# Kernel optimization log

Measured on AMD Instinct MI355X. Metric: run time of the kernel, lower is better.

The kernel has to match this reference:

```python
import jax, jax.numpy as jnp
import numpy as np
from jax import lax

HID = 128
NGRAPH = 64  # ligands per receptor


def _conv3d(x, w, b):
    # x: [N,C,D,H,W], w: [O,I,3,3,3], VALID padding (torch Conv3d default)
    y = lax.conv_general_dilated(x, w, (1, 1, 1), 'VALID',
                                 dimension_numbers=('NCDHW', 'OIDHW', 'NCDHW'))
    return y + b[None, :, None, None, None]


def setup_inputs() -> dict:
    key = jax.random.key(0)
    ks = jax.random.split(key, 40)
    i = iter(range(40))
    rn = lambda shape, s=1.0: jax.random.normal(ks[next(i)], shape, jnp.float32) * s
    W = 0.02
    inp = {
        'ms_feat_0': rn((4, 32, 16, 16, 16)),
        'ms_feat_1': rn((4, 64, 8, 8, 8)),
        'token_features': rn((4, 128, 256)),
        'lig_atom': rn((4, 1024, 64)),
        'lig_graph': rn((4, NGRAPH, 64)),
        'ligand_batch': jnp.sort(jax.random.randint(ks[next(i)], (1024,), 0, NGRAPH)).astype(jnp.int32),
        # token_mlp
        'W_token': rn((256, HID), W), 'b_token': jnp.zeros((HID,)),
        # pocket_mlp_list (reversed order: conv0 <- ms_feat_1 C=64, conv1 <- ms_feat_0 C=32)
        'Wc0': rn((HID, 64, 3, 3, 3), W), 'bc0': jnp.zeros((HID,)),
        'Wc1': rn((HID, 32, 3, 3, 3), W), 'bc1': jnp.zeros((HID,)),
        # pocket_mlp
        'W_pocket': rn((2 * HID, HID), W), 'b_pocket': jnp.zeros((HID,)),
        # concat layer / gate
        'W_cat': rn((3 * HID, HID), W), 'b_cat': jnp.zeros((HID,)),
        'W_gate': rn((3 * HID, HID), W), 'b_gate': jnp.zeros((HID,)),
        # ligand projections
        'W_atom': rn((64, HID), W), 'b_atom': jnp.zeros((HID,)),
        'W_graph': rn((64, HID), W), 'b_graph': jnp.zeros((HID,)),
        # energy bias mlp
        'W_bias1': rn((2 * HID, HID), W), 'b_bias1': jnp.zeros((HID,)),
        'W_bias2': rn((HID, 1), W), 'b_bias2': jnp.zeros((1,)),
        # interaction mlp + pair energy / gate
        'W_int': rn((HID, HID), W), 'b_int': jnp.zeros((HID,)),
        'W_pe': rn((HID, 1), W), 'b_pe': jnp.zeros((1,)),
        'W_pg': rn((HID, 1), W), 'b_pg': jnp.zeros((1,)),
    }
    return inp


def reference(ms_feat_0, ms_feat_1, token_features, lig_atom, lig_graph, ligand_batch,
              W_token, b_token, Wc0, bc0, Wc1, bc1, W_pocket, b_pocket,
              W_cat, b_cat, W_gate, b_gate, W_atom, b_atom, W_graph, b_graph,
              W_bias1, b_bias1, W_bias2, b_bias2, W_int, b_int,
              W_pe, b_pe, W_pg, b_pg):
    silu = jax.nn.silu
    lrelu = lambda x: jax.nn.leaky_relu(x, 0.01)

    # ---- ready_to_calculate ----
    # reversed multi-scale: [ms_feat_1, ms_feat_0]; SiLU -> Conv3d -> spatial mean
    p0 = _conv3d(silu(ms_feat_1), Wc0, bc0).mean(axis=(2, 3, 4))  # [N,HID]
    p1 = _conv3d(silu(ms_feat_0), Wc1, bc1).mean(axis=(2, 3, 4))  # [N,HID]
    pocket = silu(jnp.concatenate([p0, p1], -1)) @ W_pocket + b_pocket  # [N,HID]

    tok = silu(token_features) @ W_token + b_token                # [N,Nt,HID]
    tok_agg = jnp.concatenate([tok.sum(1), tok.mean(1)], -1)      # [N,2*HID]

    pf = jnp.concatenate([pocket, tok_agg], -1)                   # [N,3*HID]
    pf = (pf @ W_cat + b_cat) * jax.nn.sigmoid(pf @ W_gate + b_gate)  # [N,HID]

    # ---- per-image affinity (vectorized over images) ----
    atoms = lig_atom @ W_atom + b_atom                            # [N,Na,HID]
    # einsum('ik,jk->ijk') outer interaction map, batched over images
    imap = jnp.einsum('nik,njk->nijk', atoms, tok)                # [N,Na,Nt,HID]
    h = lrelu(imap @ W_int + b_int)                               # [N,Na,Nt,HID]
    pe = (h @ W_pe + b_pe) * jax.nn.sigmoid(h @ W_pg + b_pg)      # [N,Na,Nt,1]
    atom_e = pe.sum(axis=(2, 3))                                  # [N,Na]
    seg = jax.vmap(lambda v: jax.ops.segment_sum(v, ligand_batch, num_segments=NGRAPH))(atom_e)  # [N,Ng]

    gf = lig_graph @ W_graph + b_graph                            # [N,Ng,HID]
    pf_rep = jnp.broadcast_to(pf[:, None, :], gf.shape)           # [N,Ng,HID]
    z = jnp.concatenate([pf_rep, gf], -1)                         # [N,Ng,2*HID]
    bias = lrelu(z @ W_bias1 + b_bias1) @ W_bias2 + b_bias2       # [N,Ng,1]

    return seg + bias[..., 0]                                     # [N,Ng]
```

## Files before the change

kernel.cpp:

```cpp
#include <hip/hip_runtime.h>
#include <hip/hip_bf16.h>

#define NIMG 4

typedef __attribute__((ext_vector_type(8))) short short8v;
typedef __attribute__((ext_vector_type(4))) float float4v;

__device__ __forceinline__ float sigm(float x){ return 1.f/(1.f+__expf(-x)); }
__device__ __forceinline__ float silu(float x){ return x/(1.f+__expf(-x)); }
__device__ __forceinline__ float lrelu(float x){ return fmaxf(x, 0.01f*x); }
__device__ __forceinline__ float bf2f(unsigned short u){
  union { unsigned int i; float f; } v; v.i = ((unsigned int)u)<<16; return v.f; }
__device__ __forceinline__ unsigned short f2bf(float f){
  union { float f; unsigned int i; } v; v.f = f;
  unsigned int r = v.i + 0x7fffu + ((v.i>>16)&1u);
  return (unsigned short)(r>>16); }

__global__ void k_tok(const float* __restrict__ tf, const float* __restrict__ Wt,
                      const float* __restrict__ bt, float* __restrict__ tok,
                      float* __restrict__ toksum){
  __shared__ float sv[256];
  __shared__ float part[128];
  const int row = blockIdx.x;
  const int tid = threadIdx.x;
  const int c = tid & 127, s = tid >> 7;
  sv[tid] = silu(tf[row*256 + tid]);
  __syncthreads();
  float acc = 0.f;
  #pragma unroll 8
  for(int q=s*128; q<s*128+128; q++) acc = fmaf(sv[q], Wt[q*128+c], acc);
  if(s==1) part[c] = acc;
  __syncthreads();
  if(s==0){
    acc += part[c] + bt[c];
    tok[row*128+c] = acc;
    atomicAdd(&toksum[(row>>7)*128 + c], acc);
  }
}

template<int DIM, int ODIM>
__global__ void k_wsum(const float* __restrict__ x, float* __restrict__ S){
  __shared__ float sx[DIM*DIM*DIM];
  const float* xp = x + (size_t)blockIdx.x*(DIM*DIM*DIM);
  for(int p=threadIdx.x; p<DIM*DIM*DIM; p+=256) sx[p] = silu(xp[p]);
  __syncthreads();
  const int wave = threadIdx.x>>6, lane = threadIdx.x&63;
  for(int tap=wave; tap<27; tap+=4){
    const int kd=tap/9, kh=(tap/3)%3, kw=tap%3;
    const int base = kd*DIM*DIM + kh*DIM + kw;
    float ps = 0.f;
    for(int idx=lane; idx<ODIM*ODIM*ODIM; idx+=64){
      int od = idx/(ODIM*ODIM); int r = idx - od*(ODIM*ODIM);
      int oh = r/ODIM; int ow = r - oh*ODIM;
      ps += sx[base + od*DIM*DIM + oh*DIM + ow];
    }
    #pragma unroll
    for(int m=32;m>=1;m>>=1) ps += __shfl_xor(ps,m);
    if(lane==0) S[blockIdx.x*27 + tap] = ps;
  }
}

__global__ void k_pconv(const float* __restrict__ S1, const float* __restrict__ S0,
                        const float* __restrict__ Wc0, const float* __restrict__ bc0,
                        const float* __restrict__ Wc1, const float* __restrict__ bc1,
                        float* __restrict__ pp){
  const int b = blockIdx.x;
  const int n = b >> 7, c = b & 127;
  const int tid = threadIdx.x;
  float a0 = 0.f, a1 = 0.f;
  { const float* w = Wc0 + c*1728; const float* s = S1 + n*1728;
    for(int q=tid; q<1728; q+=256) a0 = fmaf(w[q], s[q], a0); }
  { const float* w = Wc1 + c*864;  const float* s = S0 + n*864;
    for(int q=tid; q<864; q+=256)  a1 = fmaf(w[q], s[q], a1); }
  #pragma unroll
  for(int m=32;m>=1;m>>=1){ a0 += __shfl_xor(a0,m); a1 += __shfl_xor(a1,m); }
  __shared__ float r0[4], r1[4];
  if((tid&63)==0){ r0[tid>>6]=a0; r1[tid>>6]=a1; }
  __syncthreads();
  if(tid==0){
    float p0 = bc0[c] + (r0[0]+r0[1]+r0[2]+r0[3])*(1.f/216.f);
    float p1 = bc1[c] + (r1[0]+r1[1]+r1[2]+r1[3])*(1.f/2744.f);
    pp[n*256 + c]       = silu(p0);
    pp[n*256 + 128 + c] = silu(p1);
  }
}

__global__ void k_pf2(const float* __restrict__ pp, const float* __restrict__ toksum,
                      const float* __restrict__ Wp,  const float* __restrict__ bp,
                      const float* __restrict__ Wcat, const float* __restrict__ bcat,
                      const float* __restrict__ Wgate,const float* __restrict__ bgate,
                      float* __restrict__ pf){
  __shared__ float ps[256];
  __shared__ float zz[384];
  __shared__ float part[4][128];
  __shared__ float partg[4][128];
  const int n = blockIdx.x;
  const int tid = threadIdx.x;
  const int c = tid & 127, s = tid >> 7;
  if(tid < 256) ps[tid] = pp[n*256 + tid];
  __syncthreads();
  float a = 0.f;
  for(int q=s*64; q<s*64+64; q++) a = fmaf(ps[q], Wp[q*128+c], a);
  part[s][c] = a;
  __syncthreads();
  if(s==0){
    float pk = bp[c] + part[0][c]+part[1][c]+part[2][c]+part[3][c];
    float ts = toksum[n*128+c];
    zz[c] = pk; zz[128+c] = ts; zz[256+c] = ts*(1.f/128.f);
  }
  __syncthreads();
  float a1=0.f, a2=0.f;
  for(int q=s*96; q<s*96+96; q++){
    float z = zz[q];
    a1 = fmaf(z, Wcat[q*128+c], a1);
    a2 = fmaf(z, Wgate[q*128+c], a2);
  }
  part[s][c]=a1; partg[s][c]=a2;
  __syncthreads();
  if(s==0){
    float v1 = bcat[c] +part[0][c]+part[1][c]+part[2][c]+part[3][c];
    float v2 = bgate[c]+partg[0][c]+partg[1][c]+partg[2][c]+partg[3][c];
    pf[n*128+c] = v1 * sigm(v2);
  }
}

__global__ void k_atoms(const float* __restrict__ la, const float* __restrict__ Wa,
                        const float* __restrict__ ba, unsigned short* __restrict__ atoms_bf,
                        float* __restrict__ atom_e){
  __shared__ float s[64];
  const int row = blockIdx.x;
  const int c = threadIdx.x;
  if(c < 64) s[c] = la[row*64 + c];
  __syncthreads();
  float acc = ba[c];
  #pragma unroll 8
  for(int k=0;k<64;k++) acc = fmaf(s[k], Wa[k*128+c], acc);
  atoms_bf[row*128+c] = f2bf(acc);
  if(c==0) atom_e[row] = 0.f;
}

__global__ void k_wt(const float* __restrict__ Wint, unsigned short* __restrict__ Wt){
  const int c = blockIdx.x, k = threadIdx.x;
  Wt[c*128 + k] = f2bf(Wint[k*128 + c]);
}

__global__ __launch_bounds__(512,2) void k_inter(
    const unsigned short* __restrict__ atoms_bf,
    const float* __restrict__ tok,
    const unsigned short* __restrict__ Wt,
    const float* __restrict__ bint,
    const float* __restrict__ Wpe, const float* __restrict__ bpe,
    const float* __restrict__ Wpg, const float* __restrict__ bpg,
    float* __restrict__ atom_e){
  extern __shared__ unsigned short ldsu[];
  float* red = (float*)(ldsu + 32768);

  const int b0 = blockIdx.x;
  const int bid = (b0 & 7)*64 + (b0 >> 3);
  const int n = bid >> 7;
  const int chunk = (bid >> 5) & 3;
  const int jg = bid & 31;
  const int tid = threadIdx.x;
  const int wv = tid >> 6, lane = tid & 63;
  const int q = lane >> 4, t = lane & 15;
  const int wr = wv >> 1, wc = wv & 1;

  const int rbase = n*1024 + chunk*256;

  short8v areg[4][4];
  const unsigned short* ab = atoms_bf + (size_t)rbase*128 + (wr*64 + t)*128 + q*8;
  #pragma unroll
  for(int fr=0; fr<4; fr++)
    #pragma unroll
    for(int ks=0; ks<4; ks++)
      areg[fr][ks] = *(const short8v*)(ab + fr*16*128 + ks*32);

  const int kq = (tid & 15)*8;
  const int cbb = tid >> 4;
  const int swzW = (cbb & 7) << 3;
  float wf[4][8];
  {
    short8v wtmp[4];
    #pragma unroll
    for(int i=0;i<4;i++) wtmp[i] = *(const short8v*)(Wt + (cbb + 32*i)*128 + kq);
    #pragma unroll
    for(int i=0;i<4;i++)
      #pragma unroll
      for(int e=0;e<8;e++) wf[i][e] = bf2f((unsigned short)wtmp[i][e]);
  }
  const float* tokb = tok + (size_t)(n*128 + jg*4)*128;

  float bi[4], wpe[4], wpg[4];
  #pragma unroll
  for(int fc=0; fc<4; fc++){
    int c = wc*64 + fc*16 + t;
    bi[fc] = bint[c]; wpe[fc] = Wpe[c]; wpg[fc] = Wpg[c];
  }
  const float bpe0 = bpe[0], bpg0 = bpg[0];
  const int swzB = (t & 7) << 3;

  float peacc = 0.f;

  {
    float4v t0 = *(const float4v*)(tokb + kq);
    float4v t1 = *(const float4v*)(tokb + kq + 4);
    float trv[8] = {t0[0],t0[1],t0[2],t0[3],t1[0],t1[1],t1[2],t1[3]};
    #pragma unroll
    for(int i=0;i<4;i++){
      int c = cbb + 32*i;
      short8v o;
      #pragma unroll
      for(int e=0;e<8;e++) o[e] = (short)f2bf(wf[i][e]*trv[e]);
      *(short8v*)(ldsu + (c<<7) + (kq ^ swzW)) = o;
    }
  }
  __syncthreads();

  #pragma unroll
  for(int j=0; j<4; j++){
    float trn[8];
    if(j<3){
      float4v t0 = *(const float4v*)(tokb + (j+1)*128 + kq);
      float4v t1 = *(const float4v*)(tokb + (j+1)*128 + kq + 4);
      #pragma unroll
      for(int e=0;e<4;e++){ trn[e]=t0[e]; trn[4+e]=t1[e]; }
    }
    const unsigned short* B = ldsu + (j&1)*16384;

    float4v acc[4][4];
    #pragma unroll
    for(int fr=0;fr<4;fr++)
      #pragma unroll
      for(int fc=0;fc<4;fc++)
        acc[fr][fc] = (float4v){bi[fc],bi[fc],bi[fc],bi[fc]};

    #pragma unroll
    for(int ks=0;ks<4;ks++){
      #pragma unroll
      for(int fc=0;fc<4;fc++){
        const int c = wc*64 + fc*16 + t;
        short8v bf = *(const short8v*)(B + (c<<7) + ((ks*32 + q*8) ^ swzB));
        #pragma unroll
        for(int fr=0;fr<4;fr++)
          acc[fr][fc] = __builtin_amdgcn_mfma_f32_16x16x32_bf16(areg[fr][ks], bf, acc[fr][fc], 0,0,0);
      }
    }

    #pragma unroll
    for(int fr=0;fr<4;fr++){
      #pragma unroll
      for(int r=0;r<4;r++){
        float d1=0.f, d2=0.f;
        #pragma unroll
        for(int fc=0;fc<4;fc++){
          float h = lrelu(acc[fr][fc][r]);
          d1 = fmaf(h, wpe[fc], d1);
          d2 = fmaf(h, wpg[fc], d2);
        }
        d1 += __shfl_xor(d1,1); d2 += __shfl_xor(d2,1);
        d1 += __shfl_xor(d1,2); d2 += __shfl_xor(d2,2);
        d1 += __shfl_xor(d1,4); d2 += __shfl_xor(d2,4);
        d1 += __shfl_xor(d1,8); d2 += __shfl_xor(d2,8);
        if(t==0){
          int row = wr*64 + fr*16 + q*4 + r;
          red[(wc*256 + row)*2 + 0] = d1;
          red[(wc*256 + row)*2 + 1] = d2;
        }
      }
    }
    __syncthreads();
    if(tid < 256){
      float d1 = red[tid*2]     + red[(256+tid)*2];
      float d2 = red[tid*2 + 1] + red[(256+tid)*2 + 1];
      peacc += (d1 + bpe0) * sigm(d2 + bpg0);
    }
    if(j<3){
      #pragma unroll
      for(int i=0;i<4;i++){
        int c = cbb + 32*i;
        short8v o;
        #pragma unroll
        for(int e=0;e<8;e++) o[e] = (short)f2bf(wf[i][e]*trn[e]);
        *(short8v*)(ldsu + ((j+1)&1)*16384 + (c<<7) + (kq ^ swzW)) = o;
      }
    }
    __syncthreads();
  }
  if(tid < 256) atomicAdd(atom_e + rbase + tid, peacc);
}

__global__ void k_bias_seg(const float* __restrict__ lg, const float* __restrict__ Wg,
                       const float* __restrict__ bg, const float* __restrict__ pf,
                       const float* __restrict__ W1, const float* __restrict__ b1,
                       const float* __restrict__ W2, const float* __restrict__ b2,
                       const float* __restrict__ atom_e, const int* __restrict__ batch,
                       float* __restrict__ out){
  __shared__ float row[64];
  __shared__ float z[256];
  __shared__ float red[128];
  __shared__ float red2[128];
  const int b = blockIdx.x;
  const int n = b >> 6, g = b & 63;
  const int c = threadIdx.x;
  if(c < 64) row[c] = lg[b*64 + c];
  __syncthreads();
  float gf = bg[c];
  #pragma unroll 8
  for(int k=0;k<64;k++) gf = fmaf(row[k], Wg[k*128+c], gf);
  z[c] = pf[n*128+c]; z[128+c] = gf;
  __syncthreads();
  float tacc = b1[c];
  for(int qq=0;qq<256;qq++) tacc = fmaf(z[qq], W1[qq*128+c], tacc);
  tacc = lrelu(tacc);
  float s = 0.f;
  const float* ae = atom_e + n*1024;
  for(int i=c;i<1024;i+=128){ float v = ae[i]; s += (batch[i]==g) ? v : 0.f; }
  red[c] = tacc * W2[c];
  red2[c] = s;
  __syncthreads();
  for(int st=64; st>0; st>>=1){
    if(c<st){ red[c]+=red[c+st]; red2[c]+=red2[c+st]; }
    __syncthreads();
  }
  if(c==0) out[b] = red[0] + b2[0] + red2[0];
}

extern "C" void kernel_launch(void* const* d_in, const int* in_sizes, int n_in,
                              void* d_out, int out_size, void* d_ws, size_t ws_size,
                              hipStream_t stream) {
  const float* ms0   = (const float*)d_in[0];
  const float* ms1   = (const float*)d_in[1];
  const float* tfeat = (const float*)d_in[2];
  const float* la    = (const float*)d_in[3];
  const float* lg    = (const float*)d_in[4];
  const int*   batch = (const int*)  d_in[5];
  const float* Wtok  = (const float*)d_in[6];
  const float* btok  = (const float*)d_in[7];
  const float* Wc0   = (const float*)d_in[8];
  const float* bc0   = (const float*)d_in[9];
  const float* Wc1   = (const float*)d_in[10];
  const float* bc1   = (const float*)d_in[11];
  const float* Wp    = (const float*)d_in[12];
  const float* bp    = (const float*)d_in[13];
  const float* Wcat  = (const float*)d_in[14];
  const float* bcat  = (const float*)d_in[15];
  const float* Wgate = (const float*)d_in[16];
  const float* bgate = (const float*)d_in[17];
  const float* Wa    = (const float*)d_in[18];
  const float* ba    = (const float*)d_in[19];
  const float* Wgr   = (const float*)d_in[20];
  const float* bgr   = (const float*)d_in[21];
  const float* W1    = (const float*)d_in[22];
  const float* b1    = (const float*)d_in[23];
  const float* W2    = (const float*)d_in[24];
  const float* b2    = (const float*)d_in[25];
  const float* Wint  = (const float*)d_in[26];
  const float* bint  = (const float*)d_in[27];
  const float* Wpe   = (const float*)d_in[28];
  const float* bpe   = (const float*)d_in[29];
  const float* Wpg   = (const float*)d_in[30];
  const float* bpg   = (const float*)d_in[31];
  float* out = (float*)d_out;

  float* ws      = (float*)d_ws;
  float* tok     = ws;
  float* S1      = ws + 65536;
  float* S0      = S1 + 6912;
  float* pp      = S0 + 3456;
  float* pf      = pp + 1024;
  float* toksum  = pf + 512;
  float* atom_e  = toksum + 512;
  unsigned short* atoms_bf = (unsigned short*)(atom_e + 4096);
  unsigned short* Wt       = atoms_bf + 524288;

  hipMemsetAsync(toksum, 0, 512*sizeof(float), stream);

  k_tok<<<NIMG*128, 256, 0, stream>>>(tfeat, Wtok, btok, tok, toksum);
  k_wsum<8,6><<<NIMG*64, 256, 0, stream>>>(ms1, S1);
  k_wsum<16,14><<<NIMG*32, 256, 0, stream>>>(ms0, S0);
  k_atoms<<<NIMG*1024, 128, 0, stream>>>(la, Wa, ba, atoms_bf, atom_e);
  k_wt<<<128, 128, 0, stream>>>(Wint, Wt);
  k_pconv<<<NIMG*128, 256, 0, stream>>>(S1, S0, Wc0, bc0, Wc1, bc1, pp);
  k_pf2<<<NIMG, 512, 0, stream>>>(pp, toksum, Wp, bp, Wcat, bcat, Wgate, bgate, pf);

  const int lds_bytes = 65536 + 4096;
  hipFuncSetAttribute(reinterpret_cast<const void*>(k_inter),
                      hipFuncAttributeMaxDynamicSharedMemorySize, lds_bytes);
  k_inter<<<512, 512, lds_bytes, stream>>>(atoms_bf, tok, Wt, bint,
                                           Wpe, bpe, Wpg, bpg, atom_e);

  k_bias_seg<<<NIMG*64, 128, 0, stream>>>(lg, Wgr, bgr, pf, W1, b1, W2, b2,
                                          atom_e, batch, out);
}
```

Measured before the change: 250.1 us.

## Fuse preprocessing kernels and restructure interaction GEMM to scale atom fragments in registers

The tok, wsum, atoms and weight-transpose kernels are merged into one multi-role launch, cutting launch count. The toksum atomics and memset are replaced by a direct column sum inside k_pconv. The interaction kernel no longer builds W*tok tiles in LDS with double buffering and barriers. Instead it keeps W_int fragments in registers and scales the atom A-fragments by each token using packed bf16 conversion. It also uses smaller 256-thread blocks over 64-atom by 8-token tiles and DPP row reductions. The trade-off is extra register pressure and repeated global tok loads per token.

New measurement: 215.5 us. 13.8% less time.

```diff
diff --git a/kernel.cpp b/kernel.cpp
--- a/kernel.cpp
+++ b/kernel.cpp
@@ -5,44 +5,49 @@
 
 typedef __attribute__((ext_vector_type(8))) short short8v;
 typedef __attribute__((ext_vector_type(4))) float float4v;
+typedef __attribute__((ext_vector_type(4))) int   int4v;
 
 __device__ __forceinline__ float sigm(float x){ return 1.f/(1.f+__expf(-x)); }
 __device__ __forceinline__ float silu(float x){ return x/(1.f+__expf(-x)); }
 __device__ __forceinline__ float lrelu(float x){ return fmaxf(x, 0.01f*x); }
-__device__ __forceinline__ float bf2f(unsigned short u){
-  union { unsigned int i; float f; } v; v.i = ((unsigned int)u)<<16; return v.f; }
 __device__ __forceinline__ unsigned short f2bf(float f){
   union { float f; unsigned int i; } v; v.f = f;
   unsigned int r = v.i + 0x7fffu + ((v.i>>16)&1u);
   return (unsigned short)(r>>16); }
 
-__global__ void k_tok(const float* __restrict__ tf, const float* __restrict__ Wt,
-                      const float* __restrict__ bt, float* __restrict__ tok,
-                      float* __restrict__ toksum){
-  __shared__ float sv[256];
-  __shared__ float part[128];
-  const int row = blockIdx.x;
-  const int tid = threadIdx.x;
-  const int c = tid & 127, s = tid >> 7;
-  sv[tid] = silu(tf[row*256 + tid]);
-  __syncthreads();
-  float acc = 0.f;
-  #pragma unroll 8
-  for(int q=s*128; q<s*128+128; q++) acc = fmaf(sv[q], Wt[q*128+c], acc);
-  if(s==1) part[c] = acc;
-  __syncthreads();
-  if(s==0){
-    acc += part[c] + bt[c];
-    tok[row*128+c] = acc;
-    atomicAdd(&toksum[(row>>7)*128 + c], acc);
-  }
+template<int CTRL>
+__device__ __forceinline__ float dpp_radd(float v){
+  int s = __builtin_amdgcn_update_dpp(0, __builtin_bit_cast(int, v), CTRL, 0xF, 0xF, true);
+  return v + __builtin_bit_cast(float, s);
+}
+__device__ __forceinline__ float row16_reduce(float v){
+  v = dpp_radd<0x128>(v);
+  v = dpp_radd<0x124>(v);
+  v = dpp_radd<0x122>(v);
+  v = dpp_radd<0x121>(v);
+  return v;
+}
+
+__device__ __forceinline__ short8v scale_frag(short8v a, const float* tv){
+  int4v ai = __builtin_bit_cast(int4v, a);
+  int4v oi;
+  #pragma unroll
+  for(int p=0;p<4;p++){
+    float lo = __builtin_bit_cast(float, ai[p] << 16);
+    float hi = __builtin_bit_cast(float, (int)(ai[p] & 0xFFFF0000));
+    lo *= tv[2*p]; hi *= tv[2*p+1];
+    int r;
+    asm("v_cvt_pk_bf16_f32 %0, %1, %2" : "=v"(r) : "v"(lo), "v"(hi));
+    oi[p] = r;
+  }
+  return __builtin_bit_cast(short8v, oi);
 }
 
 template<int DIM, int ODIM>
-__global__ void k_wsum(const float* __restrict__ x, float* __restrict__ S){
-  __shared__ float sx[DIM*DIM*DIM];
-  const float* xp = x + (size_t)blockIdx.x*(DIM*DIM*DIM);
-  for(int p=threadIdx.x; p<DIM*DIM*DIM; p+=256) sx[p] = silu(xp[p]);
+__device__ void wsum_body(const float* __restrict__ x, float* __restrict__ S,
+                          int vb, float* sh){
+  const float* xp = x + (size_t)vb*(DIM*DIM*DIM);
+  for(int p=threadIdx.x; p<DIM*DIM*DIM; p+=256) sh[p] = silu(xp[p]);
   __syncthreads();
   const int wave = threadIdx.x>>6, lane = threadIdx.x&63;
   for(int tap=wave; tap<27; tap+=4){
@@ -52,36 +57,86 @@
     for(int idx=lane; idx<ODIM*ODIM*ODIM; idx+=64){
       int od = idx/(ODIM*ODIM); int r = idx - od*(ODIM*ODIM);
       int oh = r/ODIM; int ow = r - oh*ODIM;
-      ps += sx[base + od*DIM*DIM + oh*DIM + ow];
+      ps += sh[base + od*DIM*DIM + oh*DIM + ow];
     }
     #pragma unroll
     for(int m=32;m>=1;m>>=1) ps += __shfl_xor(ps,m);
-    if(lane==0) S[blockIdx.x*27 + tap] = ps;
+    if(lane==0) S[vb*27 + tap] = ps;
+  }
+}
+
+__global__ __launch_bounds__(256) void k_pre(
+    const float* __restrict__ tf, const float* __restrict__ Wtok,
+    const float* __restrict__ btok, float* __restrict__ tok,
+    const float* __restrict__ ms1, float* __restrict__ S1,
+    const float* __restrict__ ms0, float* __restrict__ S0,
+    const float* __restrict__ la, const float* __restrict__ Wa,
+    const float* __restrict__ ba, unsigned short* __restrict__ atoms_bf,
+    float* __restrict__ atom_e,
+    const float* __restrict__ Wint, unsigned short* __restrict__ Wt){
+  __shared__ float sh[4096];
+  const int b = blockIdx.x;
+  const int tid = threadIdx.x;
+  if(b < 512){
+    const int row = b;
+    sh[tid] = silu(tf[row*256 + tid]);
+    __syncthreads();
+    const int c = tid & 127, sg = tid >> 7;
+    float acc = 0.f;
+    #pragma unroll 8
+    for(int q=sg*128; q<sg*128+128; q++) acc = fmaf(sh[q], Wtok[q*128+c], acc);
+    if(sg==1) sh[256+c] = acc;
+    __syncthreads();
+    if(sg==0) tok[row*128+c] = acc + sh[256+c] + btok[c];
+  } else if(b < 768){
+    wsum_body<8,6>(ms1, S1, b-512, sh);
+  } else if(b < 896){
+    wsum_body<16,14>(ms0, S0, b-768, sh);
+  } else if(b < 2944){
+    const int rowb = (b-896)*2;
+    if(tid < 128) sh[tid] = la[(size_t)rowb*64 + tid];
+    __syncthreads();
+    const int r2 = tid>>7, c = tid&127;
+    const float* s = sh + r2*64;
+    float acc = ba[c];
+    #pragma unroll 8
+    for(int k=0;k<64;k++) acc = fmaf(s[k], Wa[k*128+c], acc);
+    atoms_bf[(size_t)(rowb+r2)*128 + c] = f2bf(acc);
+    if(tid<2) atom_e[rowb+tid] = 0.f;
+  } else {
+    const int idx = (b-2944)*256 + tid;
+    const int c = idx >> 7, k = idx & 127;
+    Wt[c*128 + k] = f2bf(Wint[k*128 + c]);
   }
 }
 
 __global__ void k_pconv(const float* __restrict__ S1, const float* __restrict__ S0,
                         const float* __restrict__ Wc0, const float* __restrict__ bc0,
                         const float* __restrict__ Wc1, const float* __restrict__ bc1,
+                        const float* __restrict__ tok, float* __restrict__ toksum,
                         float* __restrict__ pp){
   const int b = blockIdx.x;
   const int n = b >> 7, c = b & 127;
   const int tid = threadIdx.x;
-  float a0 = 0.f, a1 = 0.f;
+  float a0 = 0.f, a1 = 0.f, ts = 0.f;
   { const float* w = Wc0 + c*1728; const float* s = S1 + n*1728;
     for(int q=tid; q<1728; q+=256) a0 = fmaf(w[q], s[q], a0); }
   { const float* w = Wc1 + c*864;  const float* s = S0 + n*864;
     for(int q=tid; q<864; q+=256)  a1 = fmaf(w[q], s[q], a1); }
+  for(int j=tid; j<128; j+=256) ts = tok[(n*128+j)*128 + c];
   #pragma unroll
-  for(int m=32;m>=1;m>>=1){ a0 += __shfl_xor(a0,m); a1 += __shfl_xor(a1,m); }
-  __shared__ float r0[4], r1[4];
-  if((tid&63)==0){ r0[tid>>6]=a0; r1[tid>>6]=a1; }
+  for(int m=32;m>=1;m>>=1){
+    a0 += __shfl_xor(a0,m); a1 += __shfl_xor(a1,m); ts += __shfl_xor(ts,m);
+  }
+  __shared__ float r0[4], r1[4], r2[4];
+  if((tid&63)==0){ r0[tid>>6]=a0; r1[tid>>6]=a1; r2[tid>>6]=ts; }
   __syncthreads();
   if(tid==0){
     float p0 = bc0[c] + (r0[0]+r0[1]+r0[2]+r0[3])*(1.f/216.f);
     float p1 = bc1[c] + (r1[0]+r1[1]+r1[2]+r1[3])*(1.f/2744.f);
     pp[n*256 + c]       = silu(p0);
     pp[n*256 + 128 + c] = silu(p1);
+    toksum[n*128 + c]   = r2[0]+r2[1]+r2[2]+r2[3];
   }
 }
 
@@ -124,27 +179,7 @@
   }
 }
 
-__global__ void k_atoms(const float* __restrict__ la, const float* __restrict__ Wa,
-                        const float* __restrict__ ba, unsigned short* __restrict__ atoms_bf,
-                        float* __restrict__ atom_e){
-  __shared__ float s[64];
-  const int row = blockIdx.x;
-  const int c = threadIdx.x;
-  if(c < 64) s[c] = la[row*64 + c];
-  __syncthreads();
-  float acc = ba[c];
-  #pragma unroll 8
-  for(int k=0;k<64;k++) acc = fmaf(s[k], Wa[k*128+c], acc);
-  atoms_bf[row*128+c] = f2bf(acc);
-  if(c==0) atom_e[row] = 0.f;
-}
-
-__global__ void k_wt(const float* __restrict__ Wint, unsigned short* __restrict__ Wt){
-  const int c = blockIdx.x, k = threadIdx.x;
-  Wt[c*128 + k] = f2bf(Wint[k*128 + c]);
-}
-
-__global__ __launch_bounds__(512,2) void k_inter(
+__global__ __launch_bounds__(256,2) void k_inter(
     const unsigned short* __restrict__ atoms_bf,
     const float* __restrict__ tok,
     const unsigned short* __restrict__ Wt,
@@ -152,102 +187,75 @@
     const float* __restrict__ Wpe, const float* __restrict__ bpe,
     const float* __restrict__ Wpg, const float* __restrict__ bpg,
     float* __restrict__ atom_e){
-  extern __shared__ unsigned short ldsu[];
-  float* red = (float*)(ldsu + 32768);
+  __shared__ float red[2*2*2*32*2];
 
   const int b0 = blockIdx.x;
-  const int bid = (b0 & 7)*64 + (b0 >> 3);
-  const int n = bid >> 7;
-  const int chunk = (bid >> 5) & 3;
-  const int jg = bid & 31;
+  const int bid = (b0 & 7)*128 + (b0 >> 3);
+  const int n = bid >> 8;
+  const int chunk = (bid >> 4) & 15;
+  const int jg = bid & 15;
   const int tid = threadIdx.x;
-  const int wv = tid >> 6, lane = tid & 63;
-  const int q = lane >> 4, t = lane & 15;
-  const int wr = wv >> 1, wc = wv & 1;
-
-  const int rbase = n*1024 + chunk*256;
-
-  short8v areg[4][4];
-  const unsigned short* ab = atoms_bf + (size_t)rbase*128 + (wr*64 + t)*128 + q*8;
-  #pragma unroll
-  for(int fr=0; fr<4; fr++)
-    #pragma unroll
-    for(int ks=0; ks<4; ks++)
-      areg[fr][ks] = *(const short8v*)(ab + fr*16*128 + ks*32);
-
-  const int kq = (tid & 15)*8;
-  const int cbb = tid >> 4;
-  const int swzW = (cbb & 7) << 3;
-  float wf[4][8];
-  {
-    short8v wtmp[4];
-    #pragma unroll
-    for(int i=0;i<4;i++) wtmp[i] = *(const short8v*)(Wt + (cbb + 32*i)*128 + kq);
-    #pragma unroll
-    for(int i=0;i<4;i++)
-      #pragma unroll
-      for(int e=0;e<8;e++) wf[i][e] = bf2f((unsigned short)wtmp[i][e]);
-  }
-  const float* tokb = tok + (size_t)(n*128 + jg*4)*128;
-
+  const int w = tid >> 6, lane = tid & 63;
+  const int t = lane & 15, q = lane >> 4;
+  const int g = w >> 1, wc = w & 1;
+
+  const int rbase = n*1024 + chunk*64;
+
+  short8v areg[2][4];
+  { const unsigned short* ab = atoms_bf + (size_t)(rbase + g*32 + t)*128 + q*8;
+    #pragma unroll
+    for(int fr=0;fr<2;fr++)
+      #pragma unroll
+      for(int ks=0;ks<4;ks++)
+        areg[fr][ks] = *(const short8v*)(ab + fr*16*128 + ks*32);
+  }
+  short8v breg[4][4];
+  { const unsigned short* wb = Wt + (size_t)(wc*64 + t)*128 + q*8;
+    #pragma unroll
+    for(int fc=0;fc<4;fc++)
+      #pragma unroll
+      for(int ks=0;ks<4;ks++)
+        breg[fc][ks] = *(const short8v*)(wb + fc*16*128 + ks*32);
+  }
   float bi[4], wpe[4], wpg[4];
   #pragma unroll
-  for(int fc=0; fc<4; fc++){
-    int c = wc*64 + fc*16 + t;
-    bi[fc] = bint[c]; wpe[fc] = Wpe[c]; wpg[fc] = Wpg[c];
+  for(int fc=0;fc<4;fc++){
+    int cc = wc*64 + fc*16 + t;
+    bi[fc]=bint[cc]; wpe[fc]=Wpe[cc]; wpg[fc]=Wpg[cc];
   }
   const float bpe0 = bpe[0], bpg0 = bpg[0];
-  const int swzB = (t & 7) << 3;
+  const float* tokn = tok + (size_t)(n*128 + jg*8)*128 + q*8;
 
   float peacc = 0.f;
 
-  {
-    float4v t0 = *(const float4v*)(tokb + kq);
-    float4v t1 = *(const float4v*)(tokb + kq + 4);
-    float trv[8] = {t0[0],t0[1],t0[2],t0[3],t1[0],t1[1],t1[2],t1[3]};
-    #pragma unroll
-    for(int i=0;i<4;i++){
-      int c = cbb + 32*i;
-      short8v o;
-      #pragma unroll
-      for(int e=0;e<8;e++) o[e] = (short)f2bf(wf[i][e]*trv[e]);
-      *(short8v*)(ldsu + (c<<7) + (kq ^ swzW)) = o;
-    }
-  }
-  __syncthreads();
-
-  #pragma unroll
-  for(int j=0; j<4; j++){
-    float trn[8];
-    if(j<3){
-      float4v t0 = *(const float4v*)(tokb + (j+1)*128 + kq);
-      float4v t1 = *(const float4v*)(tokb + (j+1)*128 + kq + 4);
-      #pragma unroll
-      for(int e=0;e<4;e++){ trn[e]=t0[e]; trn[4+e]=t1[e]; }
-    }
-    const unsigned short* B = ldsu + (j&1)*16384;
-
-    float4v acc[4][4];
-    #pragma unroll
-    for(int fr=0;fr<4;fr++)
+  for(int j=0;j<8;j++){
+    const int jb = j & 1;
+    float trv[4][8];
+    { const float* tr = tokn + j*128;
+      #pragma unroll
+      for(int ks=0;ks<4;ks++){
+        *(float4v*)&trv[ks][0] = *(const float4v*)(tr + ks*32);
+        *(float4v*)&trv[ks][4] = *(const float4v*)(tr + ks*32 + 4);
+      }
+    }
+    float4v acc[2][4];
+    #pragma unroll
+    for(int fr=0;fr<2;fr++)
       #pragma unroll
       for(int fc=0;fc<4;fc++)
         acc[fr][fc] = (float4v){bi[fc],bi[fc],bi[fc],bi[fc]};
-
     #pragma unroll
     for(int ks=0;ks<4;ks++){
+      short8v s0 = scale_frag(areg[0][ks], trv[ks]);
+      short8v s1 = scale_frag(areg[1][ks], trv[ks]);
       #pragma unroll
       for(int fc=0;fc<4;fc++){
-        const int c = wc*64 + fc*16 + t;
-        short8v bf = *(const short8v*)(B + (c<<7) + ((ks*32 + q*8) ^ swzB));
-        #pragma unroll
-        for(int fr=0;fr<4;fr++)
-          acc[fr][fc] = __builtin_amdgcn_mfma_f32_16x16x32_bf16(areg[fr][ks], bf, acc[fr][fc], 0,0,0);
+        acc[0][fc] = __builtin_amdgcn_mfma_f32_16x16x32_bf16(s0, breg[fc][ks], acc[0][fc], 0,0,0);
+        acc[1][fc] = __builtin_amdgcn_mfma_f32_16x16x32_bf16(s1, breg[fc][ks], acc[1][fc], 0,0,0);
       }
     }
-
-    #pragma unroll
-    for(int fr=0;fr<4;fr++){
+    #pragma unroll
+    for(int fr=0;fr<2;fr++){
       #pragma unroll
       for(int r=0;r<4;r++){
         float d1=0.f, d2=0.f;
@@ -257,36 +265,24 @@
           d1 = fmaf(h, wpe[fc], d1);
           d2 = fmaf(h, wpg[fc], d2);
         }
-        d1 += __shfl_xor(d1,1); d2 += __shfl_xor(d2,1);
-        d1 += __shfl_xor(d1,2); d2 += __shfl_xor(d2,2);
-        d1 += __shfl_xor(d1,4); d2 += __shfl_xor(d2,4);
-        d1 += __shfl_xor(d1,8); d2 += __shfl_xor(d2,8);
+        d1 = row16_reduce(d1);
+        d2 = row16_reduce(d2);
         if(t==0){
-          int row = wr*64 + fr*16 + q*4 + r;
-          red[(wc*256 + row)*2 + 0] = d1;
-          red[(wc*256 + row)*2 + 1] = d2;
+          int a = fr*16 + q*4 + r;
+          float* rp = red + (((jb*2+g)*2+wc)*32 + a)*2;
+          rp[0] = d1; rp[1] = d2;
         }
       }
     }
     __syncthreads();
-    if(tid < 256){
-      float d1 = red[tid*2]     + red[(256+tid)*2];
-      float d2 = red[tid*2 + 1] + red[(256+tid)*2 + 1];
+    if(wc==0 && lane<32){
+      const float* rp = red + (((jb*2+g)*2+0)*32 + lane)*2;
+      const float* rq = red + (((jb*2+g)*2+1)*32 + lane)*2;
+      float d1 = rp[0]+rq[0], d2 = rp[1]+rq[1];
       peacc += (d1 + bpe0) * sigm(d2 + bpg0);
     }
-    if(j<3){
-      #pragma unroll
-      for(int i=0;i<4;i++){
-        int c = cbb + 32*i;
-        short8v o;
-        #pragma unroll
-        for(int e=0;e<8;e++) o[e] = (short)f2bf(wf[i][e]*trn[e]);
-        *(short8v*)(ldsu + ((j+1)&1)*16384 + (c<<7) + (kq ^ swzW)) = o;
-      }
-    }
-    __syncthreads();
-  }
-  if(tid < 256) atomicAdd(atom_e + rbase + tid, peacc);
+  }
+  if(wc==0 && lane<32) atomicAdd(atom_e + rbase + g*32 + lane, peacc);
 }
 
 __global__ void k_bias_seg(const float* __restrict__ lg, const float* __restrict__ Wg,
@@ -373,22 +369,15 @@
   unsigned short* atoms_bf = (unsigned short*)(atom_e + 4096);
   unsigned short* Wt       = atoms_bf + 524288;
 
-  hipMemsetAsync(toksum, 0, 512*sizeof(float), stream);
-
-  k_tok<<<NIMG*128, 256, 0, stream>>>(tfeat, Wtok, btok, tok, toksum);
-  k_wsum<8,6><<<NIMG*64, 256, 0, stream>>>(ms1, S1);
-  k_wsum<16,14><<<NIMG*32, 256, 0, stream>>>(ms0, S0);
-  k_atoms<<<NIMG*1024, 128, 0, stream>>>(la, Wa, ba, atoms_bf, atom_e);
-  k_wt<<<128, 128, 0, stream>>>(Wint, Wt);
-  k_pconv<<<NIMG*128, 256, 0, stream>>>(S1, S0, Wc0, bc0, Wc1, bc1, pp);
+  k_pre<<<3008, 256, 0, stream>>>(tfeat, Wtok, btok, tok,
+                                  ms1, S1, ms0, S0,
+                                  la, Wa, ba, atoms_bf, atom_e,
+                                  Wint, Wt);
+  k_inter<<<1024, 256, 0, stream>>>(atoms_bf, tok, Wt, bint,
+                                    Wpe, bpe, Wpg, bpg, atom_e);
+  k_pconv<<<NIMG*128, 256, 0, stream>>>(S1, S0, Wc0, bc0, Wc1, bc1,
+                                        tok, toksum, pp);
   k_pf2<<<NIMG, 512, 0, stream>>>(pp, toksum, Wp, bp, Wcat, bcat, Wgate, bgate, pf);
-
-  const int lds_bytes = 65536 + 4096;
-  hipFuncSetAttribute(reinterpret_cast<const void*>(k_inter),
-                      hipFuncAttributeMaxDynamicSharedMemorySize, lds_bytes);
-  k_inter<<<512, 512, lds_bytes, stream>>>(atoms_bf, tok, Wt, bint,
-                                           Wpe, bpe, Wpg, bpg, atom_e);
-
   k_bias_seg<<<NIMG*64, 128, 0, stream>>>(lg, Wgr, bgr, pf, W1, b1, W2, b2,
                                           atom_e, batch, out);
 }
```
